# Optimization experiments

Hardware: AMD Instinct MI355X
Metric: run time of the kernel (lower is better)

Reference implementation:

```python
import jax, jax.numpy as jnp
import numpy as np

NP_, NT_, D_, E_, EP_, L_, R_ = 100000, 300000, 64, 2000000, 500000, 2, 2


def setup_inputs() -> dict:
    key = jax.random.key(0)
    ks = jax.random.split(key, 12)
    return {
        "emb_playlist": jax.random.normal(ks[0], (NP_, D_), jnp.float32),
        "emb_track": jax.random.normal(ks[1], (NT_, D_), jnp.float32),
        "W_rel": jax.random.normal(ks[2], (L_, R_, D_, D_), jnp.float32) * 0.1,
        "W_root": jax.random.normal(ks[3], (L_, D_, D_), jnp.float32) * 0.1,
        "bias": jnp.zeros((L_, D_), jnp.float32),
        "n_id_playlist": jnp.arange(NP_, dtype=jnp.int32),
        "n_id_track": jnp.arange(NT_, dtype=jnp.int32),
        "edge_pt_src": jax.random.randint(ks[4], (E_,), 0, NP_, jnp.int32),
        "edge_pt_dst": jax.random.randint(ks[5], (E_,), 0, NT_, jnp.int32),
        "edge_tp_src": jax.random.randint(ks[6], (E_,), 0, NT_, jnp.int32),
        "edge_tp_dst": jax.random.randint(ks[7], (E_,), 0, NP_, jnp.int32),
        "ell_pl": jax.random.randint(ks[8], (EP_,), 0, NP_, jnp.int32),
        "ell_tr": jax.random.randint(ks[9], (EP_,), 0, NT_, jnp.int32),
    }


def _hetero_gnn(emb_playlist, emb_track, W_rel, W_root, bias,
                n_id_playlist, n_id_track,
                edge_pt_src, edge_pt_dst, edge_tp_src, edge_tp_dst,
                ell_pl, ell_tr):
    NP = emb_playlist.shape[0]
    NT = emb_track.shape[0]
    L = W_root.shape[0]
    N = NP + NT

    # embedding lookup by n_id (identity here, but faithful gather)
    x_pl = emb_playlist[n_id_playlist]
    x_tr = emb_track[n_id_track]

    # alpha=None -> uniform 1/(L+1); buffer is softmaxed -> still uniform
    weights = jax.nn.softmax(jnp.full((L + 1,), 1.0 / (L + 1), jnp.float32))

    out_pl = x_pl * weights[0]
    out_tr = x_tr * weights[0]

    # homogeneous layout: playlists at [0, NP), tracks at [NP, NP+NT)
    x = jnp.concatenate([x_pl, x_tr], axis=0)
    rel_edges = [
        (edge_pt_src, edge_pt_dst + NP),   # playlist -> track
        (edge_tp_src + NP, edge_tp_dst),   # track -> playlist
    ]

    for i in range(L):
        # RGCNConv: root transform + per-relation mean aggregation
        h = x @ W_root[i] + bias[i]
        for r, (src, dst) in enumerate(rel_edges):
            hr = x @ W_rel[i, r]              # [N, D] transform-then-gather
            msg = hr[src]                     # [E, D]
            ssum = jax.ops.segment_sum(msg, dst, num_segments=N)
            cnt = jax.ops.segment_sum(jnp.ones_like(dst, dtype=x.dtype), dst,
                                      num_segments=N)
            h = h + ssum / jnp.maximum(cnt, 1.0)[:, None]
        x = jax.nn.relu(h)
        out_pl = out_pl + x[:NP] * weights[i + 1]
        out_tr = out_tr + x[NP:] * weights[i + 1]

    # global -> local mapping via searchsorted (faithful happy path)
    ps_idx = jnp.argsort(n_id_playlist)
    ps = n_id_playlist[ps_idx]
    pl_loc = ps_idx[jnp.clip(jnp.searchsorted(ps, ell_pl), 0, NP - 1)]
    ts_idx = jnp.argsort(n_id_track)
    ts = n_id_track[ts_idx]
    tr_loc = ts_idx[jnp.clip(jnp.searchsorted(ts, ell_tr), 0, NT - 1)]

    # dot-product link scores (dropout p=0.0 -> identity)
    return jnp.sum(out_pl[pl_loc] * out_tr[tr_loc], axis=-1)


def reference(emb_playlist, emb_track, W_rel, W_root, bias,
              n_id_playlist, n_id_track,
              edge_pt_src, edge_pt_dst, edge_tp_src, edge_tp_dst,
              ell_pl, ell_tr):
    return _hetero_gnn(emb_playlist, emb_track, W_rel, W_root, bias,
                       n_id_playlist, n_id_track,
                       edge_pt_src, edge_pt_dst, edge_tp_src, edge_tp_dst,
                       ell_pl, ell_tr)
```

## Files before the change

### kernel.cpp

```cpp
#include <hip/hip_runtime.h>
#include <stdint.h>

typedef __attribute__((ext_vector_type(8))) short bf16x8;
typedef __attribute__((ext_vector_type(4))) float f32x4;
typedef __attribute__((ext_vector_type(4))) uint32_t u32x4;

#define BN 1024
#define BNSHIFT 10
#define MAXNB 512
#define PTI 8192
#define PTHREADS 512
#define EPT (PTI / PTHREADS)

static __device__ __forceinline__ float b2f_lo(uint32_t w) {
  union { uint32_t u; float f; } c; c.u = w << 16; return c.f;
}
static __device__ __forceinline__ float b2f_hi(uint32_t w) {
  union { uint32_t u; float f; } c; c.u = w & 0xffff0000u; return c.f;
}
static __device__ __forceinline__ uint16_t f2b(float f) {
  union { float f; uint32_t u; } c; c.f = f;
  return (uint16_t)((c.u + 0x7fffu + ((c.u >> 16) & 1u)) >> 16);
}
static __device__ __forceinline__ f32x4 unpack4(uint2 t) {
  f32x4 r;
  r.x = b2f_lo(t.x); r.y = b2f_hi(t.x);
  r.z = b2f_lo(t.y); r.w = b2f_hi(t.y);
  return r;
}
static __device__ __forceinline__ void acc8(float* s, uint4 v) {
  s[0] += b2f_lo(v.x); s[1] += b2f_hi(v.x);
  s[2] += b2f_lo(v.y); s[3] += b2f_hi(v.y);
  s[4] += b2f_lo(v.z); s[5] += b2f_hi(v.z);
  s[6] += b2f_lo(v.w); s[7] += b2f_hi(v.w);
}

__global__ __launch_bounds__(256) void convert_kernel(
    const float* __restrict__ emb_pl, const float* __restrict__ emb_tr,
    uint16_t* __restrict__ xb, int NP, int N) {
  long g = (long)blockIdx.x * 256 + threadIdx.x;
  long base8 = g * 8;
  long total = (long)N * 64;
  if (base8 >= total) return;
  long plEnd = (long)NP * 64;
  const float* src = (base8 < plEnd) ? (emb_pl + base8) : (emb_tr + (base8 - plEnd));
  f32x4 a = __builtin_nontemporal_load((const f32x4*)src);
  f32x4 b = __builtin_nontemporal_load((const f32x4*)(src + 4));
  union { uint16_t h[8]; uint4 v; } o;
  o.h[0] = f2b(a.x); o.h[1] = f2b(a.y); o.h[2] = f2b(a.z); o.h[3] = f2b(a.w);
  o.h[4] = f2b(b.x); o.h[5] = f2b(b.y); o.h[6] = f2b(b.z); o.h[7] = f2b(b.w);
  *(uint4*)(xb + base8) = o.v;
}

__global__ __launch_bounds__(256) void bucket_hist_kernel(
    const int* __restrict__ pt_dst, const int* __restrict__ tp_dst,
    int* __restrict__ bucketCount, int E, int NP, int NB) {
  extern __shared__ int hist[];
  int t = threadIdx.x;
  for (int b = t; b < NB; b += 256) hist[b] = 0;
  __syncthreads();
  long total = 2L * E;
  long stride = (long)gridDim.x * 256;
  for (long e = (long)blockIdx.x * 256 + t; e < total; e += stride) {
    int dstG = (e < E) ? (NP + __builtin_nontemporal_load(&pt_dst[e]))
                       : __builtin_nontemporal_load(&tp_dst[e - E]);
    atomicAdd(&hist[dstG >> BNSHIFT], 1);
  }
  __syncthreads();
  for (int b = t; b < NB; b += 256) {
    int h = hist[b];
    if (h > 0) atomicAdd(&bucketCount[b], h);
  }
}

__global__ __launch_bounds__(1024) void bucket_scan_kernel(
    const int* __restrict__ bucketCount, int* __restrict__ bucketStart,
    int* __restrict__ gCursor, int NB) {
  __shared__ int s[1024];
  int t = threadIdx.x;
  int K = (NB + 1023) >> 10;
  int b0 = t * K;
  int local = 0;
  for (int j = 0; j < K; ++j) {
    int b = b0 + j;
    if (b < NB) local += bucketCount[b];
  }
  int acc = local;
  s[t] = local;
  __syncthreads();
  for (int off = 1; off < 1024; off <<= 1) {
    int u = (t >= off) ? s[t - off] : 0;
    __syncthreads();
    acc += u;
    s[t] = acc;
    __syncthreads();
  }
  int run = acc - local;
  for (int j = 0; j < K; ++j) {
    int b = b0 + j;
    if (b < NB) {
      bucketStart[b] = run;
      gCursor[b] = run;
      run += bucketCount[b];
    }
  }
}

__global__ __launch_bounds__(PTHREADS) void partition_kernel(
    const int* __restrict__ pt_src, const int* __restrict__ pt_dst,
    const int* __restrict__ tp_src, const int* __restrict__ tp_dst,
    int* __restrict__ gCursor, uint32_t* __restrict__ pk,
    int E, int NP, int NB) {
  __shared__ uint64_t buf[PTI];
  __shared__ int hist[MAXNB];
  __shared__ int lstart[MAXNB];
  __shared__ int gbase[MAXNB];
  __shared__ int cur[MAXNB];
  __shared__ int sc[PTHREADS];
  int t = threadIdx.x;
  long total = 2L * E;
  long e0 = (long)blockIdx.x * PTI;
  long rem = total - e0;
  int cnt = (rem < (long)PTI) ? (int)rem : PTI;

  for (int j = t; j < NB; j += PTHREADS) hist[j] = 0;
  __syncthreads();

  int bj[EPT];
  uint32_t pkj[EPT];
#pragma unroll
  for (int j = 0; j < EPT; ++j) {
    int i = j * PTHREADS + t;
    bj[j] = -1;
    if (i < cnt) {
      long e = e0 + i;
      int dstG, src;
      if (e < E) {
        dstG = NP + __builtin_nontemporal_load(&pt_dst[e]);
        src = __builtin_nontemporal_load(&pt_src[e]);
      } else {
        dstG = __builtin_nontemporal_load(&tp_dst[e - E]);
        src = NP + __builtin_nontemporal_load(&tp_src[e - E]);
      }
      int b = dstG >> BNSHIFT;
      bj[j] = b;
      pkj[j] = ((uint32_t)(dstG & (BN - 1)) << 20) | (uint32_t)src;
      atomicAdd(&hist[b], 1);
    }
  }
  __syncthreads();

  int h = (t < NB) ? hist[t] : 0;
  int acc = h;
  sc[t] = h;
  __syncthreads();
  for (int off = 1; off < PTHREADS; off <<= 1) {
    int u = (t >= off) ? sc[t - off] : 0;
    __syncthreads();
    acc += u;
    sc[t] = acc;
    __syncthreads();
  }
  if (t < NB) {
    int ls = acc - h;
    lstart[t] = ls;
    cur[t] = ls;
    gbase[t] = (h > 0) ? atomicAdd(&gCursor[t], h) : 0;
  }
  __syncthreads();

#pragma unroll
  for (int j = 0; j < EPT; ++j) {
    int b = bj[j];
    if (b >= 0) {
      int pos = atomicAdd(&cur[b], 1);
      int gpos = gbase[b] + (pos - lstart[b]);
      buf[pos] = ((uint64_t)(uint32_t)gpos << 32) | (uint64_t)pkj[j];
    }
  }
  __syncthreads();

  for (int i = t; i < cnt; i += PTHREADS) {
    uint64_t e = buf[i];
    pk[(uint32_t)(e >> 32)] = (uint32_t)e;
  }
}

__global__ __launch_bounds__(512) void local_csr_kernel(
    const int* __restrict__ bucketStart, const int* __restrict__ bucketCount,
    const uint32_t* __restrict__ pk, int* __restrict__ rowptr,
    int* __restrict__ col, int N, int TEtotal) {
  __shared__ int hist[BN];
  __shared__ int cur[BN];
  __shared__ int ssum[512];
  int t = threadIdx.x;
  int b = blockIdx.x;
  hist[t] = 0;
  hist[t + 512] = 0;
  __syncthreads();
  int beg = bucketStart[b], num = bucketCount[b];
  for (int i = t; i < num; i += 512)
    atomicAdd(&hist[__builtin_nontemporal_load(&pk[beg + i]) >> 20], 1);
  __syncthreads();
  int base0 = t * 2;
  int h0 = hist[base0], h1 = hist[base0 + 1];
  int tot = h0 + h1;
  int acc = tot;
  ssum[t] = tot;
  __syncthreads();
  for (int off = 1; off < 512; off <<= 1) {
    int u = (t >= off) ? ssum[t - off] : 0;
    __syncthreads();
    acc += u;
    ssum[t] = acc;
    __syncthreads();
  }
  int run = acc - tot;
  int ex0 = run, ex1 = run + h0;
  cur[base0] = ex0;
  cur[base0 + 1] = ex1;
  int node0 = (b << BNSHIFT) + base0;
  if (node0 < N) rowptr[node0] = beg + ex0;
  if (node0 + 1 < N) rowptr[node0 + 1] = beg + ex1;
  __syncthreads();
  for (int i = t; i < num; i += 512) {
    uint32_t w = __builtin_nontemporal_load(&pk[beg + i]);
    int dl = (int)(w >> 20);
    int pos = atomicAdd(&cur[dl], 1);
    col[beg + pos] = (int)(w & 0xFFFFFu);
  }
  if (b == 0 && t == 0) rowptr[N] = TEtotal;
}

__global__ __launch_bounds__(256) void pull_kernel(
    const int* __restrict__ rowptr, const int* __restrict__ col,
    const uint16_t* __restrict__ base, uint16_t* __restrict__ agg, int N) {
  int node = blockIdx.x * 32 + (threadIdx.x >> 3);
  int c = threadIdx.x & 7;
  if (node >= N) return;
  int beg = rowptr[node], end = rowptr[node + 1];
  float s[8] = {0, 0, 0, 0, 0, 0, 0, 0};
  const uint16_t* bp = base + c * 8;
  int i = beg;
  for (; i + 8 <= end; i += 8) {
    int cc[8];
#pragma unroll
    for (int j = 0; j < 8; ++j) cc[j] = __builtin_nontemporal_load(&col[i + j]);
    uint4 v[8];
#pragma unroll
    for (int j = 0; j < 8; ++j) v[j] = *(const uint4*)(bp + (size_t)cc[j] * 64);
#pragma unroll
    for (int j = 0; j < 8; ++j) acc8(s, v[j]);
  }
  for (; i + 4 <= end; i += 4) {
    int c0 = __builtin_nontemporal_load(&col[i]);
    int c1 = __builtin_nontemporal_load(&col[i + 1]);
    int c2 = __builtin_nontemporal_load(&col[i + 2]);
    int c3 = __builtin_nontemporal_load(&col[i + 3]);
    uint4 v0 = *(const uint4*)(bp + (size_t)c0 * 64);
    uint4 v1 = *(const uint4*)(bp + (size_t)c1 * 64);
    uint4 v2 = *(const uint4*)(bp + (size_t)c2 * 64);
    uint4 v3 = *(const uint4*)(bp + (size_t)c3 * 64);
    acc8(s, v0); acc8(s, v1); acc8(s, v2); acc8(s, v3);
  }
  for (; i < end; ++i)
    acc8(s, *(const uint4*)(bp + (size_t)__builtin_nontemporal_load(&col[i]) * 64));
  int deg = end - beg;
  float inv = 1.0f / (float)(deg > 1 ? deg : 1);
  union { uint16_t h[8]; u32x4 v; } o;
#pragma unroll
  for (int j = 0; j < 8; ++j) o.h[j] = f2b(s[j] * inv);
  __builtin_nontemporal_store(o.v, (u32x4*)(agg + (size_t)node * 64 + c * 8));
}

template <bool FUSE>
__global__ __launch_bounds__(256) void transform_kernel(
    const uint16_t* __restrict__ xpl, const uint16_t* __restrict__ xtr,
    const uint16_t* __restrict__ agg,
    const float* __restrict__ Wroot,
    const float* __restrict__ WrelP, const float* __restrict__ WrelT,
    const float* __restrict__ biasrow,
    const float* __restrict__ embP, const float* __restrict__ embT,
    uint16_t* __restrict__ xout, int NP, int NT, int BP) {
  int wave = threadIdx.x >> 6;
  int lane = threadIdx.x & 63;
  int m = lane & 15, q = lane >> 4;

  int wl, nw, ntiles, nodeBase;
  const uint16_t* xbase;
  const float* Wrel;
  const float* embBase;
  if ((int)blockIdx.x < BP) {
    wl = blockIdx.x * 4 + wave; nw = BP * 4; ntiles = NP / 16;
    xbase = xpl; Wrel = WrelP; nodeBase = 0; embBase = embP;
  } else {
    wl = (blockIdx.x - BP) * 4 + wave; nw = (gridDim.x - BP) * 4; ntiles = NT / 16;
    xbase = xtr; Wrel = WrelT; nodeBase = NP; embBase = embT;
  }

  bf16x8 br[2][4], bl[2][4];
  for (int kc = 0; kc < 2; ++kc)
    for (int ct = 0; ct < 4; ++ct) {
      int n = 16 * ct + m;
      int k0 = 32 * kc + 8 * q;
      bf16x8 t0, t1;
      for (int i = 0; i < 8; ++i) {
        t0[i] = (short)f2b(Wroot[(size_t)(k0 + i) * 64 + n]);
        t1[i] = (short)f2b(Wrel[(size_t)(k0 + i) * 64 + n]);
      }
      br[kc][ct] = t0;
      bl[kc][ct] = t1;
    }
  float bv[4];
  for (int ct = 0; ct < 4; ++ct) bv[ct] = biasrow[16 * ct + m];

  for (int t = wl; t < ntiles; t += nw) {
    int rowLocal = t * 16 + m;
    int nodeG = nodeBase + rowLocal;
    const uint16_t* xrow = xbase + (size_t)rowLocal * 64;
    bf16x8 ax0, ax1;
    if (FUSE) {
      ax0 = *(const bf16x8*)(xrow + 8 * q);
      ax1 = *(const bf16x8*)(xrow + 32 + 8 * q);
    } else {
      ax0 = __builtin_nontemporal_load((const bf16x8*)(xrow + 8 * q));
      ax1 = __builtin_nontemporal_load((const bf16x8*)(xrow + 32 + 8 * q));
    }

    const uint16_t* arow = agg + (size_t)nodeG * 64;
    bf16x8 aa0 = __builtin_nontemporal_load((const bf16x8*)(arow + 8 * q));
    bf16x8 aa1 = __builtin_nontemporal_load((const bf16x8*)(arow + 32 + 8 * q));

    f32x4 acc[4];
#pragma unroll
    for (int ct = 0; ct < 4; ++ct) acc[ct] = (f32x4){bv[ct], bv[ct], bv[ct], bv[ct]};
#pragma unroll
    for (int ct = 0; ct < 4; ++ct) {
      acc[ct] = __builtin_amdgcn_mfma_f32_16x16x32_bf16(ax0, br[0][ct], acc[ct], 0, 0, 0);
      acc[ct] = __builtin_amdgcn_mfma_f32_16x16x32_bf16(ax1, br[1][ct], acc[ct], 0, 0, 0);
      acc[ct] = __builtin_amdgcn_mfma_f32_16x16x32_bf16(aa0, bl[0][ct], acc[ct], 0, 0, 0);
      acc[ct] = __builtin_amdgcn_mfma_f32_16x16x32_bf16(aa1, bl[1][ct], acc[ct], 0, 0, 0);
    }
    int nodeRow0 = nodeBase + t * 16;
    int localRow0 = t * 16;
#pragma unroll
    for (int ct = 0; ct < 4; ++ct)
#pragma unroll
      for (int r = 0; r < 4; ++r) {
        float v = acc[ct][r];
        v = v > 0.0f ? v : 0.0f;
        int colIdx = 16 * ct + m;
        size_t go = (size_t)(nodeRow0 + 4 * q + r) * 64 + colIdx;
        if (FUSE) {
          size_t lo = (size_t)(localRow0 + 4 * q + r) * 64 + colIdx;
          float e = __builtin_nontemporal_load(&embBase[lo]);
          float x1f = b2f_lo((uint32_t)xbase[lo]);
          xout[go] = f2b(e + x1f + v);
        } else {
          xout[go] = f2b(v);
        }
      }
  }
}

__global__ void score_kernel(const int* __restrict__ ell_pl,
                             const int* __restrict__ ell_tr,
                             const uint16_t* __restrict__ S,
                             float* __restrict__ out, int EP, int NP) {
  long g = (long)blockIdx.x * blockDim.x + threadIdx.x;
  long pair = g >> 3;
  int c = (int)(g & 7);
  if (pair >= EP) return;
  int p = __builtin_nontemporal_load(&ell_pl[pair]);
  int t = __builtin_nontemporal_load(&ell_tr[pair]);
  uint4 vp = *(const uint4*)(S + (size_t)p * 64 + c * 8);
  uint4 vt = *(const uint4*)(S + (size_t)(NP + t) * 64 + c * 8);
  float partial = b2f_lo(vp.x) * b2f_lo(vt.x) + b2f_hi(vp.x) * b2f_hi(vt.x)
                + b2f_lo(vp.y) * b2f_lo(vt.y) + b2f_hi(vp.y) * b2f_hi(vt.y)
                + b2f_lo(vp.z) * b2f_lo(vt.z) + b2f_hi(vp.z) * b2f_hi(vt.z)
                + b2f_lo(vp.w) * b2f_lo(vt.w) + b2f_hi(vp.w) * b2f_hi(vt.w);
  partial += __shfl_xor(partial, 1);
  partial += __shfl_xor(partial, 2);
  partial += __shfl_xor(partial, 4);
  if (c == 0) __builtin_nontemporal_store(partial * (1.0f / 9.0f), &out[pair]);
}

extern "C" void kernel_launch(void* const* d_in, const int* in_sizes, int n_in,
                              void* d_out, int out_size, void* d_ws, size_t ws_size,
                              hipStream_t stream) {
  const float* emb_pl = (const float*)d_in[0];
  const float* emb_tr = (const float*)d_in[1];
  const float* W_rel = (const float*)d_in[2];
  const float* W_root = (const float*)d_in[3];
  const float* bias = (const float*)d_in[4];
  const int* pt_src = (const int*)d_in[7];
  const int* pt_dst = (const int*)d_in[8];
  const int* tp_src = (const int*)d_in[9];
  const int* tp_dst = (const int*)d_in[10];
  const int* ell_pl = (const int*)d_in[11];
  const int* ell_tr = (const int*)d_in[12];
  float* out = (float*)d_out;

  const int NP = in_sizes[5];
  const int NT = in_sizes[6];
  const int E = in_sizes[7];
  const int EP = in_sizes[11];
  const int N = NP + NT;
  const long TE = 2L * E;
  const int NB = (N + BN - 1) / BN;

  char* ws = (char*)d_ws;
  size_t off = 0;
  uint16_t* agg = (uint16_t*)(ws + off); off += (size_t)N * 64 * 2;
  uint16_t* x1  = (uint16_t*)(ws + off); off += (size_t)N * 64 * 2;
  uint16_t* xb0 = (uint16_t*)(ws + off); off += (size_t)N * 64 * 2;
  uint32_t* pk  = (uint32_t*)(ws + off); off += (size_t)TE * 4;
  int* col      = (int*)(ws + off);      off += (size_t)TE * 4;
  int* rowptr   = (int*)(ws + off);      off += (size_t)(N + 1) * 4;
  int* bucketCount = (int*)(ws + off);   off += (size_t)NB * 4;
  int* bucketStart = (int*)(ws + off);   off += (size_t)NB * 4;
  int* gCursor     = (int*)(ws + off);   off += (size_t)NB * 4;

  uint16_t* S = agg;

  const int TB = 256;
  long cvt = ((long)N * 64 / 8 + TB - 1) / TB;
  int pullBlocks = (N + 31) / 32;
  int scoreBlocks = (int)(((long)EP * 8 + TB - 1) / TB);
  int partBlocks = (int)((TE + PTI - 1) / PTI);
  const int BP = 256, GT = 1024;

  convert_kernel<<<(int)cvt, TB, 0, stream>>>(emb_pl, emb_tr, xb0, NP, N);

  hipMemsetAsync(bucketCount, 0, (size_t)NB * 4, stream);
  bucket_hist_kernel<<<128, TB, NB * 4, stream>>>(pt_dst, tp_dst, bucketCount,
                                                  E, NP, NB);
  bucket_scan_kernel<<<1, 1024, 0, stream>>>(bucketCount, bucketStart, gCursor, NB);
  partition_kernel<<<partBlocks, PTHREADS, 0, stream>>>(
      pt_src, pt_dst, tp_src, tp_dst, gCursor, pk, E, NP, NB);
  local_csr_kernel<<<NB, 512, 0, stream>>>(bucketStart, bucketCount, pk,
                                           rowptr, col, N, (int)TE);

  pull_kernel<<<pullBlocks, TB, 0, stream>>>(rowptr, col, xb0, agg, N);
  transform_kernel<false><<<GT, TB, 0, stream>>>(
      xb0, xb0 + (size_t)NP * 64, agg, W_root + 0 * 4096, W_rel + 1 * 4096,
      W_rel + 0 * 4096, bias + 0, nullptr, nullptr, x1, NP, NT, BP);

  pull_kernel<<<pullBlocks, TB, 0, stream>>>(rowptr, col, x1, agg, N);
  transform_kernel<true><<<GT, TB, 0, stream>>>(
      x1, x1 + (size_t)NP * 64, agg, W_root + 1 * 4096, W_rel + 3 * 4096,
      W_rel + 2 * 4096, bias + 64, emb_pl, emb_tr, S, NP, NT, BP);

  score_kernel<<<scoreBlocks, TB, 0, stream>>>(ell_pl, ell_tr, S, out, EP, NP);
}
```

Before: 606.3 us.

## Sort nodes by degree for load-balanced pull aggregation, drop nontemporal hints

Adds a counting sort of nodes by in-degree (histogram, scan, scatter into an order array). Both pull passes then process nodes in descending-degree order, so wavefront groups handle nodes of similar degree and less divergence is wasted on uneven neighbour counts. It also removes nontemporal load/store hints throughout and drops the 8-wide unrolled gather loop. The cost is three extra small kernels and a memset, plus output writes that become scattered because nodes are no longer visited in index order.

```diff
diff --git a/kernel.cpp b/kernel.cpp
--- a/kernel.cpp
+++ b/kernel.cpp
@@ -3,7 +3,6 @@
 
 typedef __attribute__((ext_vector_type(8))) short bf16x8;
 typedef __attribute__((ext_vector_type(4))) float f32x4;
-typedef __attribute__((ext_vector_type(4))) uint32_t u32x4;
 
 #define BN 1024
 #define BNSHIFT 10
@@ -11,6 +10,7 @@
 #define PTI 8192
 #define PTHREADS 512
 #define EPT (PTI / PTHREADS)
+#define DB 256
 
 static __device__ __forceinline__ float b2f_lo(uint32_t w) {
   union { uint32_t u; float f; } c; c.u = w << 16; return c.f;
@@ -21,12 +21,6 @@
 static __device__ __forceinline__ uint16_t f2b(float f) {
   union { float f; uint32_t u; } c; c.f = f;
   return (uint16_t)((c.u + 0x7fffu + ((c.u >> 16) & 1u)) >> 16);
-}
-static __device__ __forceinline__ f32x4 unpack4(uint2 t) {
-  f32x4 r;
-  r.x = b2f_lo(t.x); r.y = b2f_hi(t.x);
-  r.z = b2f_lo(t.y); r.w = b2f_hi(t.y);
-  return r;
 }
 static __device__ __forceinline__ void acc8(float* s, uint4 v) {
   s[0] += b2f_lo(v.x); s[1] += b2f_hi(v.x);
@@ -44,8 +38,8 @@
   if (base8 >= total) return;
   long plEnd = (long)NP * 64;
   const float* src = (base8 < plEnd) ? (emb_pl + base8) : (emb_tr + (base8 - plEnd));
-  f32x4 a = __builtin_nontemporal_load((const f32x4*)src);
-  f32x4 b = __builtin_nontemporal_load((const f32x4*)(src + 4));
+  f32x4 a = *(const f32x4*)src;
+  f32x4 b = *(const f32x4*)(src + 4);
   union { uint16_t h[8]; uint4 v; } o;
   o.h[0] = f2b(a.x); o.h[1] = f2b(a.y); o.h[2] = f2b(a.z); o.h[3] = f2b(a.w);
   o.h[4] = f2b(b.x); o.h[5] = f2b(b.y); o.h[6] = f2b(b.z); o.h[7] = f2b(b.w);
@@ -62,8 +56,7 @@
   long total = 2L * E;
   long stride = (long)gridDim.x * 256;
   for (long e = (long)blockIdx.x * 256 + t; e < total; e += stride) {
-    int dstG = (e < E) ? (NP + __builtin_nontemporal_load(&pt_dst[e]))
-                       : __builtin_nontemporal_load(&tp_dst[e - E]);
+    int dstG = (e < E) ? (NP + pt_dst[e]) : tp_dst[e - E];
     atomicAdd(&hist[dstG >> BNSHIFT], 1);
   }
   __syncthreads();
@@ -200,7 +193,7 @@
   __syncthreads();
   int beg = bucketStart[b], num = bucketCount[b];
   for (int i = t; i < num; i += 512)
-    atomicAdd(&hist[__builtin_nontemporal_load(&pk[beg + i]) >> 20], 1);
+    atomicAdd(&hist[pk[beg + i] >> 20], 1);
   __syncthreads();
   int base0 = t * 2;
   int h0 = hist[base0], h1 = hist[base0 + 1];
@@ -224,7 +217,7 @@
   if (node0 + 1 < N) rowptr[node0 + 1] = beg + ex1;
   __syncthreads();
   for (int i = t; i < num; i += 512) {
-    uint32_t w = __builtin_nontemporal_load(&pk[beg + i]);
+    uint32_t w = pk[beg + i];
     int dl = (int)(w >> 20);
     int pos = atomicAdd(&cur[dl], 1);
     col[beg + pos] = (int)(w & 0xFFFFFu);
@@ -232,31 +225,66 @@
   if (b == 0 && t == 0) rowptr[N] = TEtotal;
 }
 
+__global__ __launch_bounds__(DB) void deg_hist_kernel(
+    const int* __restrict__ rowptr, int* __restrict__ degCount, int N) {
+  __shared__ int h[DB];
+  int t = threadIdx.x;
+  h[t] = 0;
+  __syncthreads();
+  int stride = gridDim.x * DB;
+  for (int n = blockIdx.x * DB + t; n < N; n += stride) {
+    int d = rowptr[n + 1] - rowptr[n];
+    d = d > DB - 1 ? DB - 1 : d;
+    atomicAdd(&h[d], 1);
+  }
+  __syncthreads();
+  int v = h[t];
+  if (v > 0) atomicAdd(&degCount[t], v);
+}
+
+__global__ __launch_bounds__(DB) void deg_scatter_kernel(
+    const int* __restrict__ rowptr, int* __restrict__ degCursor,
+    int* __restrict__ order, int N, int chunk) {
+  __shared__ int h[DB];
+  __shared__ int base[DB];
+  int t = threadIdx.x;
+  int n0 = blockIdx.x * chunk;
+  int n1 = n0 + chunk;
+  if (n1 > N) n1 = N;
+  h[t] = 0;
+  __syncthreads();
+  for (int n = n0 + t; n < n1; n += DB) {
+    int d = rowptr[n + 1] - rowptr[n];
+    d = d > DB - 1 ? DB - 1 : d;
+    atomicAdd(&h[d], 1);
+  }
+  __syncthreads();
+  int v = h[t];
+  base[t] = (v > 0) ? atomicAdd(&degCursor[t], v) : 0;
+  h[t] = 0;
+  __syncthreads();
+  for (int n = n0 + t; n < n1; n += DB) {
+    int d = rowptr[n + 1] - rowptr[n];
+    d = d > DB - 1 ? DB - 1 : d;
+    int pos = base[d] + atomicAdd(&h[d], 1);
+    order[pos] = n;
+  }
+}
+
 __global__ __launch_bounds__(256) void pull_kernel(
     const int* __restrict__ rowptr, const int* __restrict__ col,
+    const int* __restrict__ order,
     const uint16_t* __restrict__ base, uint16_t* __restrict__ agg, int N) {
-  int node = blockIdx.x * 32 + (threadIdx.x >> 3);
+  int idx = blockIdx.x * 32 + (threadIdx.x >> 3);
   int c = threadIdx.x & 7;
-  if (node >= N) return;
+  if (idx >= N) return;
+  int node = order[N - 1 - idx];
   int beg = rowptr[node], end = rowptr[node + 1];
   float s[8] = {0, 0, 0, 0, 0, 0, 0, 0};
   const uint16_t* bp = base + c * 8;
   int i = beg;
-  for (; i + 8 <= end; i += 8) {
-    int cc[8];
-#pragma unroll
-    for (int j = 0; j < 8; ++j) cc[j] = __builtin_nontemporal_load(&col[i + j]);
-    uint4 v[8];
-#pragma unroll
-    for (int j = 0; j < 8; ++j) v[j] = *(const uint4*)(bp + (size_t)cc[j] * 64);
-#pragma unroll
-    for (int j = 0; j < 8; ++j) acc8(s, v[j]);
-  }
   for (; i + 4 <= end; i += 4) {
-    int c0 = __builtin_nontemporal_load(&col[i]);
-    int c1 = __builtin_nontemporal_load(&col[i + 1]);
-    int c2 = __builtin_nontemporal_load(&col[i + 2]);
-    int c3 = __builtin_nontemporal_load(&col[i + 3]);
+    int c0 = col[i], c1 = col[i + 1], c2 = col[i + 2], c3 = col[i + 3];
     uint4 v0 = *(const uint4*)(bp + (size_t)c0 * 64);
     uint4 v1 = *(const uint4*)(bp + (size_t)c1 * 64);
     uint4 v2 = *(const uint4*)(bp + (size_t)c2 * 64);
@@ -264,13 +292,13 @@
     acc8(s, v0); acc8(s, v1); acc8(s, v2); acc8(s, v3);
   }
   for (; i < end; ++i)
-    acc8(s, *(const uint4*)(bp + (size_t)__builtin_nontemporal_load(&col[i]) * 64));
+    acc8(s, *(const uint4*)(bp + (size_t)col[i] * 64));
   int deg = end - beg;
   float inv = 1.0f / (float)(deg > 1 ? deg : 1);
-  union { uint16_t h[8]; u32x4 v; } o;
+  union { uint16_t h[8]; uint4 v; } o;
 #pragma unroll
   for (int j = 0; j < 8; ++j) o.h[j] = f2b(s[j] * inv);
-  __builtin_nontemporal_store(o.v, (u32x4*)(agg + (size_t)node * 64 + c * 8));
+  *(uint4*)(agg + (size_t)node * 64 + c * 8) = o.v;
 }
 
 template <bool FUSE>
@@ -318,18 +346,12 @@
     int rowLocal = t * 16 + m;
     int nodeG = nodeBase + rowLocal;
     const uint16_t* xrow = xbase + (size_t)rowLocal * 64;
-    bf16x8 ax0, ax1;
-    if (FUSE) {
-      ax0 = *(const bf16x8*)(xrow + 8 * q);
-      ax1 = *(const bf16x8*)(xrow + 32 + 8 * q);
-    } else {
-      ax0 = __builtin_nontemporal_load((const bf16x8*)(xrow + 8 * q));
-      ax1 = __builtin_nontemporal_load((const bf16x8*)(xrow + 32 + 8 * q));
-    }
+    bf16x8 ax0 = *(const bf16x8*)(xrow + 8 * q);
+    bf16x8 ax1 = *(const bf16x8*)(xrow + 32 + 8 * q);
 
     const uint16_t* arow = agg + (size_t)nodeG * 64;
-    bf16x8 aa0 = __builtin_nontemporal_load((const bf16x8*)(arow + 8 * q));
-    bf16x8 aa1 = __builtin_nontemporal_load((const bf16x8*)(arow + 32 + 8 * q));
+    bf16x8 aa0 = *(const bf16x8*)(arow + 8 * q);
+    bf16x8 aa1 = *(const bf16x8*)(arow + 32 + 8 * q);
 
     f32x4 acc[4];
 #pragma unroll
@@ -353,7 +375,7 @@
         size_t go = (size_t)(nodeRow0 + 4 * q + r) * 64 + colIdx;
         if (FUSE) {
           size_t lo = (size_t)(localRow0 + 4 * q + r) * 64 + colIdx;
-          float e = __builtin_nontemporal_load(&embBase[lo]);
+          float e = embBase[lo];
           float x1f = b2f_lo((uint32_t)xbase[lo]);
           xout[go] = f2b(e + x1f + v);
         } else {
@@ -417,9 +439,13 @@
   uint32_t* pk  = (uint32_t*)(ws + off); off += (size_t)TE * 4;
   int* col      = (int*)(ws + off);      off += (size_t)TE * 4;
   int* rowptr   = (int*)(ws + off);      off += (size_t)(N + 1) * 4;
+  int* order    = (int*)(ws + off);      off += (size_t)N * 4;
   int* bucketCount = (int*)(ws + off);   off += (size_t)NB * 4;
   int* bucketStart = (int*)(ws + off);   off += (size_t)NB * 4;
   int* gCursor     = (int*)(ws + off);   off += (size_t)NB * 4;
+  int* degCount    = (int*)(ws + off);   off += (size_t)DB * 4;
+  int* degStart    = (int*)(ws + off);   off += (size_t)DB * 4;
+  int* degCursor   = (int*)(ws + off);   off += (size_t)DB * 4;
 
   uint16_t* S = agg;
 
@@ -428,6 +454,8 @@
   int pullBlocks = (N + 31) / 32;
   int scoreBlocks = (int)(((long)EP * 8 + TB - 1) / TB);
   int partBlocks = (int)((TE + PTI - 1) / PTI);
+  const int degBlocks = 256;
+  int degChunk = (N + degBlocks - 1) / degBlocks;
   const int BP = 256, GT = 1024;
 
   convert_kernel<<<(int)cvt, TB, 0, stream>>>(emb_pl, emb_tr, xb0, NP, N);
@@ -441,12 +469,18 @@
   local_csr_kernel<<<NB, 512, 0, stream>>>(bucketStart, bucketCount, pk,
                                            rowptr, col, N, (int)TE);
 
-  pull_kernel<<<pullBlocks, TB, 0, stream>>>(rowptr, col, xb0, agg, N);
+  hipMemsetAsync(degCount, 0, (size_t)DB * 4, stream);
+  deg_hist_kernel<<<128, DB, 0, stream>>>(rowptr, degCount, N);
+  bucket_scan_kernel<<<1, 1024, 0, stream>>>(degCount, degStart, degCursor, DB);
+  deg_scatter_kernel<<<degBlocks, DB, 0, stream>>>(rowptr, degCursor, order,
+                                                   N, degChunk);
+
+  pull_kernel<<<pullBlocks, TB, 0, stream>>>(rowptr, col, order, xb0, agg, N);
   transform_kernel<false><<<GT, TB, 0, stream>>>(
       xb0, xb0 + (size_t)NP * 64, agg, W_root + 0 * 4096, W_rel + 1 * 4096,
       W_rel + 0 * 4096, bias + 0, nullptr, nullptr, x1, NP, NT, BP);
 
-  pull_kernel<<<pullBlocks, TB, 0, stream>>>(rowptr, col, x1, agg, N);
+  pull_kernel<<<pullBlocks, TB, 0, stream>>>(rowptr, col, order, x1, agg, N);
   transform_kernel<true><<<GT, TB, 0, stream>>>(
       x1, x1 + (size_t)NP * 64, agg, W_root + 1 * 4096, W_rel + 3 * 4096,
       W_rel + 2 * 4096, bias + 64, emb_pl, emb_tr, S, NP, NT, BP);
```

Measured after the change: 586.8 us. 1.03x faster.
